# Kernel optimization log

Hardware: AMD Instinct MI355X
Metric: run time of the kernel (lower is better)

## Reference

```python
import jax, jax.numpy as jnp
import numpy as np

VOCAB, EMB, HID = 120000, 64, 128
B, T = 256, 512


def _rnn_layer(inp, W_ih, b_ih, W_hh, b_hh):
    # inp: [B,T,D]. PyTorch RNN: h_t = tanh(W_ih x_t + b_ih + W_hh h_{t-1} + b_hh)
    pre = jnp.einsum('btd,hd->bth', inp, W_ih) + b_ih + b_hh  # input part hoisted out of scan
    h0 = jnp.zeros((inp.shape[0], W_hh.shape[0]), inp.dtype)

    def step(h, p_t):
        h = jnp.tanh(p_t + h @ W_hh.T)
        return h, h

    hT, outs = jax.lax.scan(step, h0, pre.transpose(1, 0, 2))  # scan over time
    return outs.transpose(1, 0, 2), hT  # [B,T,H], [B,H]


def _layernorm(x, g, b, eps=1e-5):
    mu = jnp.mean(x, axis=-1, keepdims=True)
    var = jnp.var(x, axis=-1, keepdims=True)
    return (x - mu) * jax.lax.rsqrt(var + eps) * g + b


def setup_inputs() -> dict:
    key = jax.random.key(0)
    ks = jax.random.split(key, 10)
    emb = jax.random.normal(ks[0], (VOCAB, EMB), jnp.float32) * 0.02
    emb = emb.at[0].set(0.0)  # padding_idx=0
    s_in, s_h = 1.0 / np.sqrt(HID), 1.0 / np.sqrt(HID)
    return {
        'x': jax.random.randint(ks[1], (B, T), 0, VOCAB),
        'emb': emb,
        'W_ih1': jax.random.normal(ks[2], (HID, EMB), jnp.float32) * s_in,
        'b_ih1': jnp.zeros((HID,), jnp.float32),
        'W_hh1': jax.random.normal(ks[3], (HID, HID), jnp.float32) * s_h,
        'b_hh1': jnp.zeros((HID,), jnp.float32),
        'W_ih2': jax.random.normal(ks[4], (HID, HID), jnp.float32) * s_in,
        'b_ih2': jnp.zeros((HID,), jnp.float32),
        'W_hh2': jax.random.normal(ks[5], (HID, HID), jnp.float32) * s_h,
        'b_hh2': jnp.zeros((HID,), jnp.float32),
        'ln_g': jnp.ones((HID,), jnp.float32),
        'ln_b': jnp.zeros((HID,), jnp.float32),
        'proj_W': jax.random.normal(ks[6], (HID, HID), jnp.float32) * s_h,
        'proj_b': jnp.zeros((HID,), jnp.float32),
        'on_g': jnp.ones((HID,), jnp.float32),
        'on_b': jnp.zeros((HID,), jnp.float32),
    }


def reference(x, emb, W_ih1, b_ih1, W_hh1, b_hh1, W_ih2, b_ih2, W_hh2, b_hh2,
              ln_g, ln_b, proj_W, proj_b, on_g, on_b):
    e = emb[x]                                   # [B,T,64]
    out1, _ = _rnn_layer(e, W_ih1, b_ih1, W_hh1, b_hh1)   # dropout is identity in eval
    _, h2 = _rnn_layer(out1, W_ih2, b_ih2, W_hh2, b_hh2)  # h2: [B,128] (last hidden state)
    rep = _layernorm(h2, ln_g, ln_b)
    rep = jnp.tanh(rep @ proj_W.T + proj_b)
    rep = _layernorm(rep, on_g, on_b)
    return rep
```

## Files before the change

### kernel.cpp

```cpp
#include <hip/hip_runtime.h>

#define BT (256*512)
#define HID 128
#define EMB 64
#define CH 32

__device__ __forceinline__ float fast_tanh(float x) {
    float e = __expf(2.f * x);
    return 1.f - __fdividef(2.f, e + 1.f);
}

#define OPQ(v) asm volatile("" : "+v"(v.x), "+v"(v.y), "+v"(v.z), "+v"(v.w))

#define FMAC(a, h, w) asm("v_fmac_f32 %0, %1, %2" : "+v"(a) : "v"(h), "v"(w))
#define VMUL(a, h, w) asm("v_mul_f32 %0, %1, %2" : "=v"(a) : "v"(h), "v"(w))
#define MAC4(hc, wa, wb, wcc, wd) \
    FMAC(s0, hc, wa); FMAC(s1, hc, wb); FMAC(s2, hc, wcc); FMAC(s3, hc, wd)

#define RED_STAGE(ctrl) \
    "v_add_f32_dpp %0, %0, %0 " ctrl " row_mask:0xf bank_mask:0xf\n\t" \
    "v_add_f32_dpp %1, %1, %1 " ctrl " row_mask:0xf bank_mask:0xf\n\t" \
    "v_add_f32_dpp %2, %2, %2 " ctrl " row_mask:0xf bank_mask:0xf\n\t" \
    "v_add_f32_dpp %3, %3, %3 " ctrl " row_mask:0xf bank_mask:0xf\n\t"
#define REDUCE_L1 asm("s_nop 1\n\t" \
    RED_STAGE("quad_perm:[1,0,3,2]") \
    RED_STAGE("quad_perm:[2,3,0,1]") \
    RED_STAGE("row_half_mirror") \
    : "+v"(s0), "+v"(s1), "+v"(s2), "+v"(s3))
#define REDUCE_L2 asm("s_nop 1\n\t" \
    RED_STAGE("quad_perm:[1,0,3,2]") \
    RED_STAGE("quad_perm:[2,3,0,1]") \
    RED_STAGE("row_half_mirror") \
    RED_STAGE("row_mirror") \
    : "+v"(s0), "+v"(s1), "+v"(s2), "+v"(s3))

__global__ __launch_bounds__(256)
__attribute__((amdgpu_waves_per_eu(1, 2)))
void k_embed_pre1(
    const int* __restrict__ x, const float* __restrict__ emb,
    const float* __restrict__ Wih1, const float* __restrict__ bih1,
    const float* __restrict__ bhh1, float* __restrict__ pre1)
{
    __shared__ float sA[32][128];
    __shared__ float sW[32][132];
    __shared__ int stok[128];
    const int tid = threadIdx.x;
    const int base = blockIdx.x * 128;
    const int tx = tid & 15, ty = tid >> 4;
    const int ox = tx * 8, py = ty * 8;
    const int pl = tid & 127, half = tid >> 7;
    if (tid < 128) stok[tid] = x[base + tid];
    float acc[8][8];
#pragma unroll
    for (int p = 0; p < 8; ++p)
#pragma unroll
        for (int o = 0; o < 8; ++o) acc[p][o] = 0.f;
    __syncthreads();
    const float4* ws = (const float4*)(Wih1 + (size_t)pl * EMB + half * 16);
    const float4* as = (const float4*)(emb + (size_t)stok[pl] * EMB + half * 16);
    float4 qw[2][4], qe[2][4];
#pragma unroll
    for (int kc = 0; kc < 2; ++kc)
#pragma unroll
        for (int k = 0; k < 4; ++k) {
            qw[kc][k] = ws[kc * 8 + k];
            qe[kc][k] = as[kc * 8 + k];
        }
    for (int kc = 0; kc < 2; ++kc) {
        {
            const int jb = half * 16;
#pragma unroll
            for (int k = 0; k < 4; ++k) {
                float4 q = qw[kc][k], e = qe[kc][k];
                sW[jb + 4*k + 0][pl] = q.x; sW[jb + 4*k + 1][pl] = q.y;
                sW[jb + 4*k + 2][pl] = q.z; sW[jb + 4*k + 3][pl] = q.w;
                sA[jb + 4*k + 0][pl] = e.x; sA[jb + 4*k + 1][pl] = e.y;
                sA[jb + 4*k + 2][pl] = e.z; sA[jb + 4*k + 3][pl] = e.w;
            }
        }
        __syncthreads();
#pragma unroll 4
        for (int j = 0; j < 32; ++j) {
            float4 a0 = *(const float4*)&sA[j][py];
            float4 a1 = *(const float4*)&sA[j][py + 4];
            float4 b0 = *(const float4*)&sW[j][ox];
            float4 b1 = *(const float4*)&sW[j][ox + 4];
            float av[8] = {a0.x,a0.y,a0.z,a0.w,a1.x,a1.y,a1.z,a1.w};
            float bv[8] = {b0.x,b0.y,b0.z,b0.w,b1.x,b1.y,b1.z,b1.w};
#pragma unroll
            for (int p = 0; p < 8; ++p)
#pragma unroll
                for (int o = 0; o < 8; ++o)
                    acc[p][o] = fmaf(av[p], bv[o], acc[p][o]);
        }
        __syncthreads();
    }
    float bo[8];
#pragma unroll
    for (int o = 0; o < 8; ++o) bo[o] = bih1[ox + o] + bhh1[ox + o];
#pragma unroll
    for (int p = 0; p < 8; ++p) {
        float* cp = pre1 + (size_t)(base + py + p) * HID + ox;
        *(float4*)cp       = make_float4(acc[p][0]+bo[0], acc[p][1]+bo[1], acc[p][2]+bo[2], acc[p][3]+bo[3]);
        *(float4*)(cp + 4) = make_float4(acc[p][4]+bo[4], acc[p][5]+bo[5], acc[p][6]+bo[6], acc[p][7]+bo[7]);
    }
}

__device__ inline float bsum768(float v, volatile float* sc, int tid) {
#pragma unroll
    for (int off = 32; off > 0; off >>= 1) v += __shfl_down(v, off, 64);
    __syncthreads();
    if ((tid & 63) == 0) sc[tid >> 6] = v;
    __syncthreads();
    float s = 0.f;
#pragma unroll
    for (int k = 0; k < 12; ++k) s += sc[k];
    return s;
}

__global__ __launch_bounds__(768)
__attribute__((amdgpu_waves_per_eu(3)))
void k_rnn_fused(
    const float* __restrict__ pre1, const float* __restrict__ Whh1,
    const float* __restrict__ Wih2, const float* __restrict__ bih2,
    const float* __restrict__ bhh2, const float* __restrict__ Whh2,
    const float* __restrict__ ln_g, const float* __restrict__ ln_b,
    const float* __restrict__ projW, const float* __restrict__ proj_b,
    const float* __restrict__ on_g, const float* __restrict__ on_b,
    float* __restrict__ out)
{
    __shared__ __align__(16) float h1[2][160];
    __shared__ __align__(16) float h2[2][160];
    __shared__ __align__(16) float spre[CH * HID];
    __shared__ float sfin[HID];
    __shared__ float sc[12];

    const int bb   = blockIdx.x;
    const int tid  = threadIdx.x;
    const int w    = tid >> 6;
    const int lane = tid & 63;
    const bool L1  = (w < 4);
    const int  e   = lane & 7;
    const int  m   = L1 ? 0 : ((lane >> 3) & 1);
    const int  rg  = L1 ? (lane >> 3) : (lane >> 4);
    const int  rowbase = L1 ? (32 * w + rg) : (16 * (w - 4) + rg);
    const int  rstep   = L1 ? 8 : 4;
    const float* wmat  = L1 ? Whh1 : (m ? Whh2 : Wih2);

    const float4* wr0 = (const float4*)(wmat + (size_t)(rowbase            ) * HID + e * 16);
    const float4* wr1 = (const float4*)(wmat + (size_t)(rowbase +     rstep) * HID + e * 16);
    const float4* wr2 = (const float4*)(wmat + (size_t)(rowbase + 2 * rstep) * HID + e * 16);
    const float4* wr3 = (const float4*)(wmat + (size_t)(rowbase + 3 * rstep) * HID + e * 16);
    float4 w0 = wr0[0], w1 = wr0[1], w2  = wr0[2], w3  = wr0[3],
           w4 = wr1[0], w5 = wr1[1], w6  = wr1[2], w7  = wr1[3],
           w8 = wr2[0], w9 = wr2[1], w10 = wr2[2], w11 = wr2[3],
           w12= wr3[0], w13= wr3[1], w14 = wr3[2], w15 = wr3[3];
    OPQ(w0);OPQ(w1);OPQ(w2);OPQ(w3);OPQ(w4);OPQ(w5);OPQ(w6);OPQ(w7);
    OPQ(w8);OPQ(w9);OPQ(w10);OPQ(w11);OPQ(w12);OPQ(w13);OPQ(w14);OPQ(w15);

    const bool wr_en = L1 ? (e < 4) : (m == 0 && e < 4);
    const int  wrow  = rowbase + (e & 3) * rstep;
    const int  wword = ((wrow >> 4) * 20) + (wrow & 15);
    const float b2w  = (!L1 && wr_en) ? (bih2[wrow] + bhh2[wrow]) : 0.f;

    if (tid < 160) { h1[0][tid] = 0.f; h2[0][tid] = 0.f; }

    const float* srcb = (L1 || m == 0) ? &h1[0][0] : &h2[0][0];
    const float4* rp0 = (const float4*)(srcb + e * 20);
    const float4* rp1 = (const float4*)(srcb + 160 + e * 20);
    float* dstb = L1 ? &h1[0][0] : &h2[0][0];
    float* wp_e = dstb + 160 + wword;
    float* wp_o = dstb + wword;

    const float4* gsrc = (const float4*)(pre1 + (size_t)bb * 512 * HID);
    float4* spv = (float4*)spre;
    float4 pf0, pf1;
    if (tid < 512) { pf0 = gsrc[tid]; pf1 = gsrc[tid + 512]; }
    __syncthreads();

    auto do_step = [&](int t, const float* spp, const float4* rp, float* wpt) {
        float4 hv0 = rp[0], hv1 = rp[1], hv2 = rp[2], hv3 = rp[3];
        float s0, s1, s2, s3;
        VMUL(s0, hv0.x, w0.x); VMUL(s1, hv0.x, w4.x);
        VMUL(s2, hv0.x, w8.x); VMUL(s3, hv0.x, w12.x);
        MAC4(hv0.y, w0.y, w4.y, w8.y, w12.y);
        MAC4(hv0.z, w0.z, w4.z, w8.z, w12.z);
        MAC4(hv0.w, w0.w, w4.w, w8.w, w12.w);
        MAC4(hv1.x, w1.x, w5.x, w9.x, w13.x);
        MAC4(hv1.y, w1.y, w5.y, w9.y, w13.y);
        MAC4(hv1.z, w1.z, w5.z, w9.z, w13.z);
        MAC4(hv1.w, w1.w, w5.w, w9.w, w13.w);
        MAC4(hv2.x, w2.x, w6.x, w10.x, w14.x);
        MAC4(hv2.y, w2.y, w6.y, w10.y, w14.y);
        MAC4(hv2.z, w2.z, w6.z, w10.z, w14.z);
        MAC4(hv2.w, w2.w, w6.w, w10.w, w14.w);
        MAC4(hv3.x, w3.x, w7.x, w11.x, w15.x);
        MAC4(hv3.y, w3.y, w7.y, w11.y, w15.y);
        MAC4(hv3.z, w3.z, w7.z, w11.z, w15.z);
        MAC4(hv3.w, w3.w, w7.w, w11.w, w15.w);
        if (L1) { REDUCE_L1; } else { REDUCE_L2; }
        if (wr_en) {
            float ta = (e & 1) ? s1 : s0;
            float tb = (e & 1) ? s3 : s2;
            float v  = (e & 2) ? tb : ta;
            if (L1) *wpt = fast_tanh(spp[wrow] + v);
            else    *wpt = (t > 0) ? fast_tanh(b2w + v) : 0.f;
        }
        __syncthreads();
    };

#pragma unroll 1
    for (int c = 0; c < 512 / CH; ++c) {
        if (tid < 512) { spv[tid] = pf0; spv[tid + 512] = pf1; }
        __syncthreads();
        if (c < 512 / CH - 1 && tid < 512) {
            pf0 = gsrc[(c + 1) * 1024 + tid];
            pf1 = gsrc[(c + 1) * 1024 + tid + 512];
        }
        const int t0 = c * CH;
        const float* spp = spre;
#pragma unroll 1
        for (int s = 0; s < CH; s += 2) {
            do_step(t0 + s,     spp,       rp0, wp_e);
            do_step(t0 + s + 1, spp + HID, rp1, wp_o);
            spp += 2 * HID;
        }
    }

    {
        float* wpD = L1 ? wp_e : &sfin[wrow];
        do_step(512, spre, rp0, wpD);
    }

    const int i = tid & 127;
    float hn = (tid < 128) ? sfin[i] : 0.f;
    float s1v = bsum768(hn, sc, tid);
    float s2v = bsum768(hn * hn, sc, tid);
    float mu = s1v * (1.f / 128.f);
    float var = s2v * (1.f / 128.f) - mu * mu;
    __syncthreads();
    if (tid < 128) spre[i] = (hn - mu) * rsqrtf(var + 1e-5f) * ln_g[i] + ln_b[i];
    __syncthreads();
    float pv = 0.f;
    if (tid < 128) {
        float a0 = proj_b[i], a1 = 0, a2 = 0, a3 = 0;
        const float4* hp = (const float4*)spre;
        const float4* pr = (const float4*)(projW + (size_t)i * HID);
#pragma unroll
        for (int k = 0; k < HID / 4; ++k) {
            float4 u = pr[k];
            float4 hv = hp[k];
            a0 = fmaf(hv.x, u.x, a0); a1 = fmaf(hv.y, u.y, a1);
            a2 = fmaf(hv.z, u.z, a2); a3 = fmaf(hv.w, u.w, a3);
        }
        pv = tanhf((a0 + a1) + (a2 + a3));
    }
    float t1 = bsum768(pv, sc, tid);
    float t2 = bsum768(pv * pv, sc, tid);
    float mu2 = t1 * (1.f / 128.f);
    float var2 = t2 * (1.f / 128.f) - mu2 * mu2;
    if (tid < 128)
        out[(size_t)bb * HID + i] = (pv - mu2) * rsqrtf(var2 + 1e-5f) * on_g[i] + on_b[i];
}

extern "C" void kernel_launch(void* const* d_in, const int* in_sizes, int n_in,
                              void* d_out, int out_size, void* d_ws, size_t ws_size,
                              hipStream_t stream)
{
    const int*   x     = (const int*)  d_in[0];
    const float* emb   = (const float*)d_in[1];
    const float* Wih1  = (const float*)d_in[2];
    const float* bih1  = (const float*)d_in[3];
    const float* Whh1  = (const float*)d_in[4];
    const float* bhh1  = (const float*)d_in[5];
    const float* Wih2  = (const float*)d_in[6];
    const float* bih2  = (const float*)d_in[7];
    const float* Whh2  = (const float*)d_in[8];
    const float* bhh2  = (const float*)d_in[9];
    const float* ln_g  = (const float*)d_in[10];
    const float* ln_b  = (const float*)d_in[11];
    const float* projW = (const float*)d_in[12];
    const float* projb = (const float*)d_in[13];
    const float* on_g  = (const float*)d_in[14];
    const float* on_b  = (const float*)d_in[15];

    float* pre1 = (float*)d_ws;

    k_embed_pre1<<<BT / 128, 256, 0, stream>>>(x, emb, Wih1, bih1, bhh1, pre1);
    k_rnn_fused<<<256, 768, 0, stream>>>(pre1, Whh1, Wih2, bih2, bhh2, Whh2,
                                         ln_g, ln_b, projW, projb, on_g, on_b,
                                         (float*)d_out);
}
```

Baseline: 438.0 us.

## Precompute input projection over vocabulary and gather per-step from table

```diff
diff --git a/kernel.cpp b/kernel.cpp
--- a/kernel.cpp
+++ b/kernel.cpp
@@ -1,9 +1,8 @@
 #include <hip/hip_runtime.h>
 
-#define BT (256*512)
 #define HID 128
 #define EMB 64
-#define CH 32
+#define VOCAB 120000
 
 __device__ __forceinline__ float fast_tanh(float x) {
     float e = __expf(2.f * x);
@@ -36,28 +35,26 @@
 
 __global__ __launch_bounds__(256)
 __attribute__((amdgpu_waves_per_eu(1, 2)))
-void k_embed_pre1(
-    const int* __restrict__ x, const float* __restrict__ emb,
-    const float* __restrict__ Wih1, const float* __restrict__ bih1,
-    const float* __restrict__ bhh1, float* __restrict__ pre1)
+void k_w1e(
+    const float* __restrict__ emb, const float* __restrict__ Wih1,
+    const float* __restrict__ bih1, const float* __restrict__ bhh1,
+    float* __restrict__ W1E)
 {
     __shared__ float sA[32][128];
     __shared__ float sW[32][132];
-    __shared__ int stok[128];
     const int tid = threadIdx.x;
     const int base = blockIdx.x * 128;
     const int tx = tid & 15, ty = tid >> 4;
     const int ox = tx * 8, py = ty * 8;
     const int pl = tid & 127, half = tid >> 7;
-    if (tid < 128) stok[tid] = x[base + tid];
+    const int rv = min(base + pl, VOCAB - 1);
     float acc[8][8];
 #pragma unroll
     for (int p = 0; p < 8; ++p)
 #pragma unroll
         for (int o = 0; o < 8; ++o) acc[p][o] = 0.f;
-    __syncthreads();
     const float4* ws = (const float4*)(Wih1 + (size_t)pl * EMB + half * 16);
-    const float4* as = (const float4*)(emb + (size_t)stok[pl] * EMB + half * 16);
+    const float4* as = (const float4*)(emb + (size_t)rv * EMB + half * 16);
     float4 qw[2][4], qe[2][4];
 #pragma unroll
     for (int kc = 0; kc < 2; ++kc)
@@ -100,9 +97,12 @@
     for (int o = 0; o < 8; ++o) bo[o] = bih1[ox + o] + bhh1[ox + o];
 #pragma unroll
     for (int p = 0; p < 8; ++p) {
-        float* cp = pre1 + (size_t)(base + py + p) * HID + ox;
-        *(float4*)cp       = make_float4(acc[p][0]+bo[0], acc[p][1]+bo[1], acc[p][2]+bo[2], acc[p][3]+bo[3]);
-        *(float4*)(cp + 4) = make_float4(acc[p][4]+bo[4], acc[p][5]+bo[5], acc[p][6]+bo[6], acc[p][7]+bo[7]);
+        const int vout = base + py + p;
+        if (vout < VOCAB) {
+            float* cp = W1E + (size_t)vout * HID + ox;
+            *(float4*)cp       = make_float4(acc[p][0]+bo[0], acc[p][1]+bo[1], acc[p][2]+bo[2], acc[p][3]+bo[3]);
+            *(float4*)(cp + 4) = make_float4(acc[p][4]+bo[4], acc[p][5]+bo[5], acc[p][6]+bo[6], acc[p][7]+bo[7]);
+        }
     }
 }
 
@@ -121,7 +121,8 @@
 __global__ __launch_bounds__(768)
 __attribute__((amdgpu_waves_per_eu(3)))
 void k_rnn_fused(
-    const float* __restrict__ pre1, const float* __restrict__ Whh1,
+    const int* __restrict__ x, const float* __restrict__ W1E,
+    const float* __restrict__ Whh1,
     const float* __restrict__ Wih2, const float* __restrict__ bih2,
     const float* __restrict__ bhh2, const float* __restrict__ Whh2,
     const float* __restrict__ ln_g, const float* __restrict__ ln_b,
@@ -131,8 +132,9 @@
 {
     __shared__ __align__(16) float h1[2][160];
     __shared__ __align__(16) float h2[2][160];
-    __shared__ __align__(16) float spre[CH * HID];
+    __shared__ int   tok[512];
     __shared__ float sfin[HID];
+    __shared__ float xn[HID];
     __shared__ float sc[12];
 
     const int bb   = blockIdx.x;
@@ -162,8 +164,10 @@
     const int  wrow  = rowbase + (e & 3) * rstep;
     const int  wword = ((wrow >> 4) * 20) + (wrow & 15);
     const float b2w  = (!L1 && wr_en) ? (bih2[wrow] + bhh2[wrow]) : 0.f;
+    const bool pfe   = L1 && wr_en;
 
     if (tid < 160) { h1[0][tid] = 0.f; h2[0][tid] = 0.f; }
+    if (tid < 512) tok[tid] = x[bb * 512 + tid];
 
     const float* srcb = (L1 || m == 0) ? &h1[0][0] : &h2[0][0];
     const float4* rp0 = (const float4*)(srcb + e * 20);
@@ -172,13 +176,16 @@
     float* wp_e = dstb + 160 + wword;
     float* wp_o = dstb + wword;
 
-    const float4* gsrc = (const float4*)(pre1 + (size_t)bb * 512 * HID);
-    float4* spv = (float4*)spre;
-    float4 pf0, pf1;
-    if (tid < 512) { pf0 = gsrc[tid]; pf1 = gsrc[tid + 512]; }
-    __syncthreads();
-
-    auto do_step = [&](int t, const float* spp, const float4* rp, float* wpt) {
+    __syncthreads();
+
+    float pA = 0.f, pB = 0.f;
+    if (pfe) {
+        pA = W1E[(size_t)tok[0] * HID + wrow];
+        pB = W1E[(size_t)tok[1] * HID + wrow];
+    }
+
+    auto do_step = [&](int t, float& pslot, int tn, const float4* rp, float* wpt) {
+        const float pv = pslot;
         float4 hv0 = rp[0], hv1 = rp[1], hv2 = rp[2], hv3 = rp[3];
         float s0, s1, s2, s3;
         VMUL(s0, hv0.x, w0.x); VMUL(s1, hv0.x, w4.x);
@@ -199,37 +206,26 @@
         MAC4(hv3.z, w3.z, w7.z, w11.z, w15.z);
         MAC4(hv3.w, w3.w, w7.w, w11.w, w15.w);
         if (L1) { REDUCE_L1; } else { REDUCE_L2; }
+        if (pfe) pslot = W1E[(size_t)tok[tn] * HID + wrow];
         if (wr_en) {
             float ta = (e & 1) ? s1 : s0;
             float tb = (e & 1) ? s3 : s2;
             float v  = (e & 2) ? tb : ta;
-            if (L1) *wpt = fast_tanh(spp[wrow] + v);
+            if (L1) *wpt = fast_tanh(pv + v);
             else    *wpt = (t > 0) ? fast_tanh(b2w + v) : 0.f;
         }
         __syncthreads();
     };
 
 #pragma unroll 1
-    for (int c = 0; c < 512 / CH; ++c) {
-        if (tid < 512) { spv[tid] = pf0; spv[tid + 512] = pf1; }
-        __syncthreads();
-        if (c < 512 / CH - 1 && tid < 512) {
-            pf0 = gsrc[(c + 1) * 1024 + tid];
-            pf1 = gsrc[(c + 1) * 1024 + tid + 512];
-        }
-        const int t0 = c * CH;
-        const float* spp = spre;
-#pragma unroll 1
-        for (int s = 0; s < CH; s += 2) {
-            do_step(t0 + s,     spp,       rp0, wp_e);
-            do_step(t0 + s + 1, spp + HID, rp1, wp_o);
-            spp += 2 * HID;
-        }
+    for (int t = 0; t < 512; t += 2) {
+        do_step(t,     pA, (t + 2 < 512) ? t + 2 : 511, rp0, wp_e);
+        do_step(t + 1, pB, (t + 3 < 512) ? t + 3 : 511, rp1, wp_o);
     }
 
     {
         float* wpD = L1 ? wp_e : &sfin[wrow];
-        do_step(512, spre, rp0, wpD);
+        do_step(512, pA, 511, rp0, wpD);
     }
 
     const int i = tid & 127;
@@ -239,12 +235,12 @@
     float mu = s1v * (1.f / 128.f);
     float var = s2v * (1.f / 128.f) - mu * mu;
     __syncthreads();
-    if (tid < 128) spre[i] = (hn - mu) * rsqrtf(var + 1e-5f) * ln_g[i] + ln_b[i];
+    if (tid < 128) xn[i] = (hn - mu) * rsqrtf(var + 1e-5f) * ln_g[i] + ln_b[i];
     __syncthreads();
     float pv = 0.f;
     if (tid < 128) {
         float a0 = proj_b[i], a1 = 0, a2 = 0, a3 = 0;
-        const float4* hp = (const float4*)spre;
+        const float4* hp = (const float4*)xn;
         const float4* pr = (const float4*)(projW + (size_t)i * HID);
 #pragma unroll
         for (int k = 0; k < HID / 4; ++k) {
@@ -284,10 +280,10 @@
     const float* on_g  = (const float*)d_in[14];
     const float* on_b  = (const float*)d_in[15];
 
-    float* pre1 = (float*)d_ws;
-
-    k_embed_pre1<<<BT / 128, 256, 0, stream>>>(x, emb, Wih1, bih1, bhh1, pre1);
-    k_rnn_fused<<<256, 768, 0, stream>>>(pre1, Whh1, Wih2, bih2, bhh2, Whh2,
+    float* W1E = (float*)d_ws;
+
+    k_w1e<<<(VOCAB + 127) / 128, 256, 0, stream>>>(emb, Wih1, bih1, bhh1, W1E);
+    k_rnn_fused<<<256, 768, 0, stream>>>(x, W1E, Whh1, Wih2, bih2, bhh2, Whh2,
                                          ln_g, ln_b, projW, projb, on_g, on_b,
                                          (float*)d_out);
 }
```

Result: no change. 433.6 us (-1.0%).
